# Performance work log

Measured on AMD Instinct MI355X. Metric: run time of the kernel, lower is better.

Reference implementation:

```python
import jax, jax.numpy as jnp
import numpy as np

N, L, I, H, D = 8192, 8, 256, 512, 8
PER = N // D  # nodes per depth level; level 0 nodes are tree roots


def setup_inputs() -> dict:
    key = jax.random.key(0)
    ks = jax.random.split(key, 9)
    s = 0.05
    x_seq = jax.random.normal(ks[0], (N, L, I), jnp.float32)
    # GRU params (torch nn.GRU layout, gate order r,z,n), stored transposed [in, 3H]
    W_ih = jax.random.normal(ks[1], (I, 3 * H), jnp.float32) * s
    W_hh = jax.random.normal(ks[2], (H, 3 * H), jnp.float32) * s
    b_ih = jax.random.normal(ks[3], (3 * H,), jnp.float32) * s
    b_hh = jax.random.normal(ks[4], (3 * H,), jnp.float32) * s
    # Child-sum TreeLSTM params: x-projections for i,o,u,f and recurrent U's
    Wx = jax.random.normal(ks[5], (H, 4 * H), jnp.float32) * s
    bx = jax.random.normal(ks[6], (4 * H,), jnp.float32) * s
    U_iou = jax.random.normal(ks[7], (H, 3 * H), jnp.float32) * s
    U_f = jax.random.normal(ks[8], (H, H), jnp.float32) * s
    # Forest structure: D levels of PER nodes; node at level d>0 has a random
    # parent at level d-1; roots (level 0) point at themselves (contribution is
    # zero because their own state is still zero when level 0 is processed).
    rng = np.random.default_rng(0)
    depth = np.repeat(np.arange(D), PER).astype(np.int32)
    parent = np.arange(N, dtype=np.int32)
    for d in range(1, D):
        parent[d * PER:(d + 1) * PER] = rng.integers((d - 1) * PER, d * PER, PER)
    root_ids = np.arange(PER, dtype=np.int32)
    return {
        "x_seq": x_seq, "W_ih": W_ih, "W_hh": W_hh, "b_ih": b_ih, "b_hh": b_hh,
        "Wx": Wx, "bx": bx, "U_iou": U_iou, "U_f": U_f,
        "parent": jnp.asarray(parent), "depth": jnp.asarray(depth),
        "root_ids": jnp.asarray(root_ids), "n_levels": D,
    }


def reference(x_seq, W_ih, W_hh, b_ih, b_hh, Wx, bx, U_iou, U_f,
              parent, depth, root_ids, n_levels):
    n = x_seq.shape[0]
    h_dim = W_hh.shape[0]

    # --- GRU over each node's encoding sequence (all nodes batched) ---
    def gru_step(h, x_t):  # h: [N,H], x_t: [N,I]
        gi = x_t @ W_ih + b_ih
        gh = h @ W_hh + b_hh
        ir, iz, inn = jnp.split(gi, 3, axis=-1)
        hr, hz, hn = jnp.split(gh, 3, axis=-1)
        r = jax.nn.sigmoid(ir + hr)
        z = jax.nn.sigmoid(iz + hz)
        ng = jnp.tanh(inn + r * hn)
        return (1.0 - z) * ng + z * h, None

    h0 = jnp.zeros((n, h_dim), x_seq.dtype)
    enc, _ = jax.lax.scan(gru_step, h0, jnp.swapaxes(x_seq, 0, 1))  # [N,H]

    # --- Child-sum TreeLSTM, processed leaves -> roots by depth level ---
    xg = enc @ Wx + bx  # [N,4H]
    xi, xo, xu, xf = jnp.split(xg, 4, axis=-1)
    c = jnp.zeros((n, h_dim), x_seq.dtype)
    h = jnp.zeros((n, h_dim), x_seq.dtype)
    for level in range(n_levels - 1, -1, -1):
        h_sum = jax.ops.segment_sum(h, parent, num_segments=n)  # sum over children
        giou = h_sum @ U_iou
        i = jax.nn.sigmoid(xi + giou[:, :h_dim])
        o = jax.nn.sigmoid(xo + giou[:, h_dim:2 * h_dim])
        u = jnp.tanh(xu + giou[:, 2 * h_dim:])
        # per-child forget gate uses parent's x projection and child's h
        f = jax.nn.sigmoid(xf[parent] + h @ U_f)
        fc = jax.ops.segment_sum(f * c, parent, num_segments=n)
        c_new = i * u + fc
        mask = (depth == level)[:, None]
        c = jnp.where(mask, c_new, c)
        h = jnp.where(mask, o * jnp.tanh(c_new), h)

    # root states per tree, stacked as [2, n_trees, H] -> (c_root, h_root)
    return jnp.stack([c[root_ids], h[root_ids]])
```

## Files before the change

kernel.cpp:

```cpp
#include <hip/hip_runtime.h>
#include <math.h>

typedef short bf16x8 __attribute__((ext_vector_type(8)));
typedef float f32x4 __attribute__((ext_vector_type(4)));

__device__ __forceinline__ float sigf(float x) { return 1.0f / (1.0f + __expf(-x)); }

__device__ __forceinline__ unsigned short f2bf(float f) {
    union { float f; unsigned u; } v; v.f = f;
    unsigned r = (v.u + 0x7FFFu + ((v.u >> 16) & 1u)) >> 16;
    return (unsigned short)r;
}
__device__ __forceinline__ float bf2f(unsigned short u) {
    union { unsigned u; float f; } v; v.u = ((unsigned)u) << 16; return v.f;
}

__device__ __forceinline__ void gload16(const unsigned short* g, unsigned short* l) {
    __builtin_amdgcn_global_load_lds(
        (const __attribute__((address_space(1))) void*)g,
        (__attribute__((address_space(3))) void*)l, 16, 0, 0);
}

__device__ __forceinline__ int swz(int slot, int row) {
    return (slot ^ ((row >> 1) & 3)) * 8;
}

__global__ void cvt_f32_bf16(const float* __restrict__ src,
                             unsigned short* __restrict__ dst, int n)
{
    const int i = (blockIdx.x * blockDim.x + threadIdx.x) * 4;
    if (i >= n) return;
    const float4 v = *reinterpret_cast<const float4*>(src + i);
    ushort4 o;
    o.x = f2bf(v.x); o.y = f2bf(v.y); o.z = f2bf(v.z); o.w = f2bf(v.w);
    *reinterpret_cast<ushort4*>(dst + i) = o;
}

__global__ void transpose_cvt(const float* __restrict__ src,
                              unsigned short* __restrict__ dst,
                              int rows, int cols)
{
    __shared__ float tile[32][33];
    const int bc = blockIdx.x * 32, br = blockIdx.y * 32;
    const int tx = threadIdx.x, ty = threadIdx.y;
    #pragma unroll
    for (int i = 0; i < 32; i += 8)
        tile[ty + i][tx] = src[(size_t)(br + ty + i) * cols + bc + tx];
    __syncthreads();
    #pragma unroll
    for (int i = 0; i < 32; i += 8)
        dst[(size_t)(bc + ty + i) * rows + br + tx] = f2bf(tile[tx][ty + i]);
}

__global__ __launch_bounds__(256)
void gru_mfma(const unsigned short* __restrict__ xb, int t,
              const unsigned short* __restrict__ hbi,
              unsigned short* __restrict__ hbo,
              const unsigned short* __restrict__ WihT,
              const unsigned short* __restrict__ WhhT,
              const float* __restrict__ b_ih, const float* __restrict__ b_hh)
{
    constexpr int I = 256, H = 512, LI = 2048;
    const int m0 = blockIdx.x * 128, j0 = blockIdx.y * 64;
    const int tid = (int)threadIdx.x, lane = tid & 63, wid = tid >> 6;
    const int wm = wid >> 1, wn = wid & 1;
    const int fr = lane & 15, kg = lane >> 4;
    const int lrow = lane >> 2;
    const int scol = swz(lane & 3, lrow);

    __shared__ unsigned short smem[3 * 10240];

    f32x4 ar[4][2], az[4][2], an[4][2], ah[4][2];
    #pragma unroll
    for (int i = 0; i < 4; ++i)
        #pragma unroll
        for (int j = 0; j < 2; ++j) {
            ar[i][j] = (f32x4){0.f, 0.f, 0.f, 0.f};
            az[i][j] = (f32x4){0.f, 0.f, 0.f, 0.f};
            an[i][j] = (f32x4){0.f, 0.f, 0.f, 0.f};
            ah[i][j] = (f32x4){0.f, 0.f, 0.f, 0.f};
        }

    constexpr int nkt1 = I / 32;
    constexpr int nkt = (I + H) / 32;

    auto stage = [&](int buf, int kt) {
        const bool s1 = (kt < nkt1);
        const int k0 = s1 ? kt * 32 : (kt - nkt1) * 32;
        unsigned short* base = &smem[buf * 10240];
        #pragma unroll
        for (int q = 0; q < 5; ++q) {
            const int c = wid * 5 + q;
            if (c < 8) {
                const int row = c * 16 + lrow;
                const unsigned short* g = s1
                    ? xb + (size_t)(m0 + row) * LI + t * I + k0 + scol
                    : hbi + (size_t)(m0 + row) * H + k0 + scol;
                gload16(g, base + c * 512);
            } else {
                const int bc = c - 8, gi = bc >> 2;
                const int row = (bc & 3) * 16 + lrow;
                const unsigned short* g = s1
                    ? WihT + (size_t)(gi * H + j0 + row) * I + k0 + scol
                    : WhhT + (size_t)(gi * H + j0 + row) * H + k0 + scol;
                gload16(g, base + c * 512);
            }
        }
    };

    stage(0, 0); stage(1, 1); stage(2, 2);
    int cur = 0;

    for (int kt = 0; kt < nkt; ++kt) {
        if (kt + 2 < nkt)      asm volatile("s_waitcnt vmcnt(10)" ::: "memory");
        else if (kt + 1 < nkt) asm volatile("s_waitcnt vmcnt(5)" ::: "memory");
        else                   asm volatile("s_waitcnt vmcnt(0)" ::: "memory");
        __builtin_amdgcn_s_barrier();

        const unsigned short* sb = &smem[cur * 10240];
        bf16x8 af[4], bfr[2], bfz[2], bfn[2];
        #pragma unroll
        for (int mi = 0; mi < 4; ++mi) {
            const int row = wm * 64 + mi * 16 + fr;
            af[mi] = *reinterpret_cast<const bf16x8*>(&sb[row * 32 + swz(kg, row)]);
        }
        #pragma unroll
        for (int ni = 0; ni < 2; ++ni) {
            const int row = wn * 32 + ni * 16 + fr;
            const int sw = swz(kg, row);
            bfr[ni] = *reinterpret_cast<const bf16x8*>(&sb[4096 + row * 32 + sw]);
            bfz[ni] = *reinterpret_cast<const bf16x8*>(&sb[4096 + (64 + row) * 32 + sw]);
            bfn[ni] = *reinterpret_cast<const bf16x8*>(&sb[4096 + (128 + row) * 32 + sw]);
        }
        const bool p1 = (kt < nkt1);
        #pragma unroll
        for (int mi = 0; mi < 4; ++mi)
            #pragma unroll
            for (int ni = 0; ni < 2; ++ni) {
                ar[mi][ni] = __builtin_amdgcn_mfma_f32_16x16x32_bf16(af[mi], bfr[ni], ar[mi][ni], 0, 0, 0);
                az[mi][ni] = __builtin_amdgcn_mfma_f32_16x16x32_bf16(af[mi], bfz[ni], az[mi][ni], 0, 0, 0);
                if (p1)
                    an[mi][ni] = __builtin_amdgcn_mfma_f32_16x16x32_bf16(af[mi], bfn[ni], an[mi][ni], 0, 0, 0);
                else
                    ah[mi][ni] = __builtin_amdgcn_mfma_f32_16x16x32_bf16(af[mi], bfn[ni], ah[mi][ni], 0, 0, 0);
            }

        asm volatile("s_waitcnt lgkmcnt(0)" ::: "memory");
        __builtin_amdgcn_s_barrier();
        if (kt + 3 < nkt) stage(cur, kt + 3);
        cur = (cur == 2) ? 0 : cur + 1;
    }

    #pragma unroll
    for (int ni = 0; ni < 2; ++ni) {
        const int j = j0 + wn * 32 + ni * 16 + fr;
        const float bir = b_ih[j],         bhr = b_hh[j];
        const float biz = b_ih[H + j],     bhz = b_hh[H + j];
        const float bin = b_ih[2 * H + j], bhn = b_hh[2 * H + j];
        #pragma unroll
        for (int mi = 0; mi < 4; ++mi) {
            #pragma unroll
            for (int r = 0; r < 4; ++r) {
                const int m = m0 + wm * 64 + mi * 16 + kg * 4 + r;
                const float rg = sigf(ar[mi][ni][r] + bir + bhr);
                const float zg = sigf(az[mi][ni][r] + biz + bhz);
                const float ng = tanhf(an[mi][ni][r] + bin + rg * (ah[mi][ni][r] + bhn));
                const size_t off = (size_t)m * H + j;
                const float hv = bf2f(hbi[off]);
                hbo[off] = f2bf((1.f - zg) * ng + zg * hv);
            }
        }
    }
}

__global__ __launch_bounds__(256)
void mfma_gemm128(const unsigned short* __restrict__ A,
                  const unsigned short* __restrict__ BT,
                  const float* __restrict__ bias,
                  float* __restrict__ C, int M, int N, int K)
{
    const int m0 = blockIdx.x * 128, n0 = blockIdx.y * 128;
    const int tid = (int)threadIdx.x, lane = tid & 63, wid = tid >> 6;
    const int wm = wid >> 1, wn = wid & 1;
    const int fr = lane & 15, kg = lane >> 4;
    const int lrow = lane >> 2;
    const int scol = swz(lane & 3, lrow);

    __shared__ unsigned short smem[3 * 8192];

    f32x4 acc[4][4];
    #pragma unroll
    for (int i = 0; i < 4; ++i)
        #pragma unroll
        for (int j = 0; j < 4; ++j)
            acc[i][j] = (f32x4){0.f, 0.f, 0.f, 0.f};

    auto stage = [&](int buf, int kt) {
        const int k0 = kt * 32;
        unsigned short* base = &smem[buf * 8192];
        #pragma unroll
        for (int q = 0; q < 4; ++q) {
            const int c = wid * 4 + q;
            const unsigned short* g = (c < 8)
                ? A + (size_t)(m0 + c * 16 + lrow) * K + k0 + scol
                : BT + (size_t)(n0 + (c - 8) * 16 + lrow) * K + k0 + scol;
            gload16(g, base + c * 512);
        }
    };

    const int nkt = K >> 5;
    stage(0, 0); stage(1, 1); stage(2, 2);
    int cur = 0;

    for (int kt = 0; kt < nkt; ++kt) {
        if (kt + 2 < nkt)      asm volatile("s_waitcnt vmcnt(8)" ::: "memory");
        else if (kt + 1 < nkt) asm volatile("s_waitcnt vmcnt(4)" ::: "memory");
        else                   asm volatile("s_waitcnt vmcnt(0)" ::: "memory");
        __builtin_amdgcn_s_barrier();

        const unsigned short* sb = &smem[cur * 8192];
        bf16x8 af[4], bf[4];
        #pragma unroll
        for (int mi = 0; mi < 4; ++mi) {
            const int row = wm * 64 + mi * 16 + fr;
            af[mi] = *reinterpret_cast<const bf16x8*>(&sb[row * 32 + swz(kg, row)]);
        }
        #pragma unroll
        for (int ni = 0; ni < 4; ++ni) {
            const int row = wn * 64 + ni * 16 + fr;
            bf[ni] = *reinterpret_cast<const bf16x8*>(&sb[4096 + row * 32 + swz(kg, row)]);
        }
        #pragma unroll
        for (int mi = 0; mi < 4; ++mi)
            #pragma unroll
            for (int ni = 0; ni < 4; ++ni)
                acc[mi][ni] = __builtin_amdgcn_mfma_f32_16x16x32_bf16(
                    af[mi], bf[ni], acc[mi][ni], 0, 0, 0);

        asm volatile("s_waitcnt lgkmcnt(0)" ::: "memory");
        __builtin_amdgcn_s_barrier();
        if (kt + 3 < nkt) stage(cur, kt + 3);
        cur = (cur == 2) ? 0 : cur + 1;
    }

    #pragma unroll
    for (int ni = 0; ni < 4; ++ni) {
        const int n = n0 + wn * 64 + ni * 16 + fr;
        const float bv = bias ? bias[n] : 0.f;
        #pragma unroll
        for (int mi = 0; mi < 4; ++mi)
            #pragma unroll
            for (int r = 0; r < 4; ++r) {
                const int m = m0 + wm * 64 + mi * 16 + kg * 4 + r;
                C[(size_t)m * N + n] = acc[mi][ni][r] + bv;
            }
    }
}

__global__ __launch_bounds__(256)
void tree_gemm(const unsigned short* __restrict__ hTb,
               const unsigned short* __restrict__ UcombT,
               const float* __restrict__ xg,
               const float* __restrict__ cT,
               const int* __restrict__ parent,
               int cstart, int pstart,
               float* __restrict__ giou,
               float* __restrict__ fcs)
{
    constexpr int H = 512, N4H = 2048, G3H = 1536;
    const int m0 = blockIdx.x * 64, n0 = blockIdx.y * 128;
    const int tid = (int)threadIdx.x, lane = tid & 63, wid = tid >> 6;
    const int wm = wid >> 1, wn = wid & 1;
    const int fr = lane & 15, kg = lane >> 4;
    const int lrow = lane >> 2;
    const int scol = swz(lane & 3, lrow);

    __shared__ unsigned short smem[3 * 6144];

    f32x4 acc[2][4];
    #pragma unroll
    for (int i = 0; i < 2; ++i)
        #pragma unroll
        for (int j = 0; j < 4; ++j)
            acc[i][j] = (f32x4){0.f, 0.f, 0.f, 0.f};

    auto stage = [&](int buf, int kt) {
        const int k0 = kt * 32;
        unsigned short* base = &smem[buf * 6144];
        #pragma unroll
        for (int q = 0; q < 3; ++q) {
            const int c = wid * 3 + q;
            const unsigned short* g = (c < 4)
                ? hTb + (size_t)(cstart + m0 + c * 16 + lrow) * H + k0 + scol
                : UcombT + (size_t)(n0 + (c - 4) * 16 + lrow) * H + k0 + scol;
            gload16(g, base + c * 512);
        }
    };

    constexpr int nkt = H / 32;
    stage(0, 0); stage(1, 1); stage(2, 2);
    int cur = 0;

    for (int kt = 0; kt < nkt; ++kt) {
        if (kt + 2 < nkt)      asm volatile("s_waitcnt vmcnt(6)" ::: "memory");
        else if (kt + 1 < nkt) asm volatile("s_waitcnt vmcnt(3)" ::: "memory");
        else                   asm volatile("s_waitcnt vmcnt(0)" ::: "memory");
        __builtin_amdgcn_s_barrier();

        const unsigned short* sb = &smem[cur * 6144];
        bf16x8 af[2], bf[4];
        #pragma unroll
        for (int mi = 0; mi < 2; ++mi) {
            const int row = wm * 32 + mi * 16 + fr;
            af[mi] = *reinterpret_cast<const bf16x8*>(&sb[row * 32 + swz(kg, row)]);
        }
        #pragma unroll
        for (int ni = 0; ni < 4; ++ni) {
            const int row = wn * 64 + ni * 16 + fr;
            bf[ni] = *reinterpret_cast<const bf16x8*>(&sb[2048 + row * 32 + swz(kg, row)]);
        }
        #pragma unroll
        for (int mi = 0; mi < 2; ++mi)
            #pragma unroll
            for (int ni = 0; ni < 4; ++ni)
                acc[mi][ni] = __builtin_amdgcn_mfma_f32_16x16x32_bf16(
                    af[mi], bf[ni], acc[mi][ni], 0, 0, 0);

        asm volatile("s_waitcnt lgkmcnt(0)" ::: "memory");
        __builtin_amdgcn_s_barrier();
        if (kt + 3 < nkt) stage(cur, kt + 3);
        cur = (cur == 2) ? 0 : cur + 1;
    }

    if (n0 < G3H) {
        #pragma unroll
        for (int mi = 0; mi < 2; ++mi)
            #pragma unroll
            for (int r = 0; r < 4; ++r) {
                const int m = m0 + wm * 32 + mi * 16 + kg * 4 + r;
                const int p = parent[cstart + m] - pstart;
                #pragma unroll
                for (int ni = 0; ni < 4; ++ni) {
                    const int n = n0 + wn * 64 + ni * 16 + fr;
                    atomicAdd(&giou[(size_t)p * G3H + n], acc[mi][ni][r]);
                }
            }
    } else {
        #pragma unroll
        for (int mi = 0; mi < 2; ++mi)
            #pragma unroll
            for (int r = 0; r < 4; ++r) {
                const int m = m0 + wm * 32 + mi * 16 + kg * 4 + r;
                const int child = cstart + m;
                const int p = parent[child];
                #pragma unroll
                for (int ni = 0; ni < 4; ++ni) {
                    const int jf = n0 + wn * 64 + ni * 16 + fr - G3H;
                    const float f = sigf(acc[mi][ni][r] + xg[(size_t)p * N4H + G3H + jf]);
                    atomicAdd(&fcs[(size_t)(p - pstart) * H + jf],
                              f * cT[(size_t)child * H + jf]);
                }
            }
    }
}

__global__ void level_update(const float* __restrict__ xg,
                             float* __restrict__ giou,
                             float* __restrict__ fcs,
                             float* __restrict__ cT, float* __restrict__ hT,
                             unsigned short* __restrict__ hb, int pstart)
{
    constexpr int H = 512, N4H = 2048, G3H = 1536;
    const int idx = blockIdx.x * blockDim.x + threadIdx.x;
    const int pi = idx >> 9, j = idx & (H - 1);
    const int p = pstart + pi;
    const size_t xb4 = (size_t)p * N4H;
    const size_t gb = (size_t)pi * G3H;
    const float ig = sigf(xg[xb4 + j] + giou[gb + j]);
    const float og = sigf(xg[xb4 + H + j] + giou[gb + H + j]);
    const float ug = tanhf(xg[xb4 + 2 * H + j] + giou[gb + 2 * H + j]);
    const float cn = ig * ug + fcs[idx];
    const float hn = og * tanhf(cn);
    const size_t off = (size_t)p * H + j;
    cT[off] = cn;
    hT[off] = hn;
    hb[off] = f2bf(hn);
    giou[gb + j] = 0.f;
    giou[gb + H + j] = 0.f;
    giou[gb + 2 * H + j] = 0.f;
    fcs[idx] = 0.f;
}

__global__ void gather_out_kernel(const float* __restrict__ c,
                                  const float* __restrict__ h,
                                  const int* __restrict__ root_ids,
                                  int nroot, float* __restrict__ out)
{
    constexpr int H = 512;
    const int idx = blockIdx.x * blockDim.x + threadIdx.x;
    const int t = idx >> 9, j = idx & (H - 1);
    const int rid = root_ids[t];
    out[idx] = c[(size_t)rid * H + j];
    out[(size_t)nroot * H + idx] = h[(size_t)rid * H + j];
}

extern "C" void kernel_launch(void* const* d_in, const int* in_sizes, int n_in,
                              void* d_out, int out_size, void* d_ws, size_t ws_size,
                              hipStream_t stream)
{
    const float* x_seq = (const float*)d_in[0];
    const float* W_ih  = (const float*)d_in[1];
    const float* W_hh  = (const float*)d_in[2];
    const float* b_ih  = (const float*)d_in[3];
    const float* b_hh  = (const float*)d_in[4];
    const float* Wx    = (const float*)d_in[5];
    const float* bx    = (const float*)d_in[6];
    const float* U_iou = (const float*)d_in[7];
    const float* U_f   = (const float*)d_in[8];
    const int* parent  = (const int*)d_in[9];
    const int* root_ids = (const int*)d_in[11];

    const int threeH = in_sizes[3];
    const int H   = threeH / 3;
    const int I   = in_sizes[1] / threeH;
    const int N   = in_sizes[9];
    const int L   = in_sizes[0] / (N * I);
    const int PER = in_sizes[11];
    const int D   = N / PER;

    const size_t NH = (size_t)N * H;
    const size_t PH = (size_t)PER * H;

    char* p = (char*)d_ws;
    const size_t zone_sz = ((size_t)N * 4 * H * 4 > (size_t)N * L * I * 2)
                         ? (size_t)N * 4 * H * 4 : (size_t)N * L * I * 2;
    unsigned short* xb = (unsigned short*)p;
    float* xg = (float*)p;                       p += zone_sz;
    unsigned short* hb0 = (unsigned short*)p;    p += NH * 2;
    unsigned short* hb1 = (unsigned short*)p;    p += NH * 2;
    float* cT = (float*)p;                       p += NH * 4;
    float* hT = (float*)p;                       p += NH * 4;
    unsigned short* WihT = (unsigned short*)p;   p += (size_t)threeH * I * 2;
    unsigned short* WhhT = (unsigned short*)p;   p += (size_t)threeH * H * 2;
    unsigned short* WxT  = (unsigned short*)p;   p += (size_t)4 * H * H * 2;
    unsigned short* UcombT = (unsigned short*)p; p += (size_t)4 * H * H * 2;
    float* giou = (float*)p;                     p += PH * 3 * 4;
    float* fcs  = (float*)p;                     p += PH * 4;
    if ((size_t)(p - (char*)d_ws) > ws_size) return;

    {
        const int n = N * L * I;
        cvt_f32_bf16<<<(n / 4 + 255) / 256, 256, 0, stream>>>(x_seq, xb, n);
        dim3 blk(32, 8);
        transpose_cvt<<<dim3(threeH / 32, I / 32), blk, 0, stream>>>(W_ih, WihT, I, threeH);
        transpose_cvt<<<dim3(threeH / 32, H / 32), blk, 0, stream>>>(W_hh, WhhT, H, threeH);
        transpose_cvt<<<dim3(4 * H / 32, H / 32), blk, 0, stream>>>(Wx, WxT, H, 4 * H);
        transpose_cvt<<<dim3(threeH / 32, H / 32), blk, 0, stream>>>(U_iou, UcombT, H, threeH);
        transpose_cvt<<<dim3(H / 32, H / 32), blk, 0, stream>>>(
            U_f, UcombT + (size_t)threeH * H, H, H);
    }
    hipMemsetAsync(hb0, 0, NH * 2, stream);
    hipMemsetAsync(giou, 0, PH * 4 * 4, stream);

    {
        dim3 grid(N / 128, H / 64);
        for (int t = 0; t < L; ++t) {
            const unsigned short* hin = (t & 1) ? hb1 : hb0;
            unsigned short* hout = (t & 1) ? hb0 : hb1;
            gru_mfma<<<grid, 256, 0, stream>>>(xb, t, hin, hout,
                                               WihT, WhhT, b_ih, b_hh);
        }
    }

    mfma_gemm128<<<dim3(N / 128, 4 * H / 128), 256, 0, stream>>>(
        hb0, WxT, bx, xg, N, 4 * H, H);

    unsigned short* hTb = hb1;
    const int pw_blocks = (int)(PH / 256);

    for (int lvl = D - 1; lvl >= 0; --lvl) {
        const int pstart = lvl * PER;
        const int cstart = (lvl + 1) * PER;

        if (lvl < D - 1)
            tree_gemm<<<dim3(PER / 64, (4 * H) / 128), 256, 0, stream>>>(
                hTb, UcombT, xg, cT, parent, cstart, pstart, giou, fcs);

        level_update<<<pw_blocks, 256, 0, stream>>>(xg, giou, fcs, cT, hT,
                                                    hTb, pstart);
    }

    gather_out_kernel<<<pw_blocks, 256, 0, stream>>>(cT, hT, root_ids, PER,
                                                     (float*)d_out);
}
```

Before: 541.5 us.

## Fuse GRU timesteps and tree levels into persistent kernels with grid barriers

The eight per-timestep GRU launches become one persistent kernel that loops over time. Blocks synchronize through a software grid barrier built on atomics, and the first input tiles for the next step are prefetched before the barrier. The per-level tree GEMM, level update and root gather are likewise merged into one persistent 256-block kernel with grid barriers between phases. Fast exp/rcp-based sigmoid and tanh replace the library calls. This removes about two dozen kernel launches and their gaps, but correctness now depends on every block being resident at once, and the fast tanh is slightly less accurate.

```diff
diff --git a/kernel.cpp b/kernel.cpp
--- a/kernel.cpp
+++ b/kernel.cpp
@@ -4,7 +4,13 @@
 typedef short bf16x8 __attribute__((ext_vector_type(8)));
 typedef float f32x4 __attribute__((ext_vector_type(4)));
 
-__device__ __forceinline__ float sigf(float x) { return 1.0f / (1.0f + __expf(-x)); }
+__device__ __forceinline__ float sigf(float x) {
+    return __builtin_amdgcn_rcpf(1.f + __expf(-x));
+}
+__device__ __forceinline__ float tanhf_fast(float x) {
+    const float e = __expf(2.f * x);
+    return 1.f - 2.f * __builtin_amdgcn_rcpf(e + 1.f);
+}
 
 __device__ __forceinline__ unsigned short f2bf(float f) {
     union { float f; unsigned u; } v; v.f = f;
@@ -23,6 +29,24 @@
 
 __device__ __forceinline__ int swz(int slot, int row) {
     return (slot ^ ((row >> 1) & 3)) * 8;
+}
+
+__device__ __forceinline__ void grid_sync(unsigned* cnt, unsigned* gen,
+                                          unsigned nb, unsigned my)
+{
+    __syncthreads();
+    if (threadIdx.x == 0) {
+        __threadfence();
+        if (atomicAdd(cnt, 1u) == nb - 1u) {
+            atomicExch(cnt, 0u);
+            __threadfence();
+            atomicExch(gen, my + 1u);
+        } else {
+            while (atomicAdd(gen, 0u) <= my) __builtin_amdgcn_s_sleep(2);
+        }
+        __threadfence();
+    }
+    __syncthreads();
 }
 
 __global__ void cvt_f32_bf16(const float* __restrict__ src,
@@ -52,16 +76,18 @@
         dst[(size_t)(bc + ty + i) * rows + br + tx] = f2bf(tile[tx][ty + i]);
 }
 
-__global__ __launch_bounds__(256)
-void gru_mfma(const unsigned short* __restrict__ xb, int t,
-              const unsigned short* __restrict__ hbi,
-              unsigned short* __restrict__ hbo,
-              const unsigned short* __restrict__ WihT,
-              const unsigned short* __restrict__ WhhT,
-              const float* __restrict__ b_ih, const float* __restrict__ b_hh)
+__global__ __launch_bounds__(256, 2)
+void gru_fused(const unsigned short* __restrict__ xb,
+               const unsigned short* __restrict__ WihT,
+               const unsigned short* __restrict__ WhhT,
+               const float* __restrict__ b_ih, const float* __restrict__ b_hh,
+               unsigned short* __restrict__ hb0,
+               unsigned short* __restrict__ hb1,
+               int L, unsigned* __restrict__ bar)
 {
     constexpr int I = 256, H = 512, LI = 2048;
-    const int m0 = blockIdx.x * 128, j0 = blockIdx.y * 64;
+    const int bx = blockIdx.x;
+    const int m0 = (bx >> 3) * 128, j0 = (bx & 7) * 64;
     const int tid = (int)threadIdx.x, lane = tid & 63, wid = tid >> 6;
     const int wm = wid >> 1, wn = wid & 1;
     const int fr = lane & 15, kg = lane >> 4;
@@ -70,21 +96,12 @@
 
     __shared__ unsigned short smem[3 * 10240];
 
-    f32x4 ar[4][2], az[4][2], an[4][2], ah[4][2];
-    #pragma unroll
-    for (int i = 0; i < 4; ++i)
-        #pragma unroll
-        for (int j = 0; j < 2; ++j) {
-            ar[i][j] = (f32x4){0.f, 0.f, 0.f, 0.f};
-            az[i][j] = (f32x4){0.f, 0.f, 0.f, 0.f};
-            an[i][j] = (f32x4){0.f, 0.f, 0.f, 0.f};
-            ah[i][j] = (f32x4){0.f, 0.f, 0.f, 0.f};
-        }
-
     constexpr int nkt1 = I / 32;
     constexpr int nkt = (I + H) / 32;
 
-    auto stage = [&](int buf, int kt) {
+    const unsigned short* hbi = hb0;
+
+    auto stage = [&](int buf, int kt, int tt) {
         const bool s1 = (kt < nkt1);
         const int k0 = s1 ? kt * 32 : (kt - nkt1) * 32;
         unsigned short* base = &smem[buf * 10240];
@@ -94,7 +111,7 @@
             if (c < 8) {
                 const int row = c * 16 + lrow;
                 const unsigned short* g = s1
-                    ? xb + (size_t)(m0 + row) * LI + t * I + k0 + scol
+                    ? xb + (size_t)(m0 + row) * LI + tt * I + k0 + scol
                     : hbi + (size_t)(m0 + row) * H + k0 + scol;
                 gload16(g, base + c * 512);
             } else {
@@ -108,68 +125,91 @@
         }
     };
 
-    stage(0, 0); stage(1, 1); stage(2, 2);
-    int cur = 0;
-
-    for (int kt = 0; kt < nkt; ++kt) {
-        if (kt + 2 < nkt)      asm volatile("s_waitcnt vmcnt(10)" ::: "memory");
-        else if (kt + 1 < nkt) asm volatile("s_waitcnt vmcnt(5)" ::: "memory");
-        else                   asm volatile("s_waitcnt vmcnt(0)" ::: "memory");
-        __builtin_amdgcn_s_barrier();
-
-        const unsigned short* sb = &smem[cur * 10240];
-        bf16x8 af[4], bfr[2], bfz[2], bfn[2];
-        #pragma unroll
-        for (int mi = 0; mi < 4; ++mi) {
-            const int row = wm * 64 + mi * 16 + fr;
-            af[mi] = *reinterpret_cast<const bf16x8*>(&sb[row * 32 + swz(kg, row)]);
-        }
+    stage(0, 0, 0); stage(1, 1, 0); stage(2, 2, 0);
+
+    for (int t = 0; t < L; ++t) {
+        hbi = (t & 1) ? hb1 : hb0;
+        unsigned short* hbo = (t & 1) ? hb0 : hb1;
+
+        f32x4 ar[4][2], az[4][2], an[4][2], ah[4][2];
+        #pragma unroll
+        for (int i = 0; i < 4; ++i)
+            #pragma unroll
+            for (int j = 0; j < 2; ++j) {
+                ar[i][j] = (f32x4){0.f, 0.f, 0.f, 0.f};
+                az[i][j] = (f32x4){0.f, 0.f, 0.f, 0.f};
+                an[i][j] = (f32x4){0.f, 0.f, 0.f, 0.f};
+                ah[i][j] = (f32x4){0.f, 0.f, 0.f, 0.f};
+            }
+
+        int cur = 0;
+        for (int kt = 0; kt < nkt; ++kt) {
+            if (kt + 2 < nkt)      asm volatile("s_waitcnt vmcnt(10)" ::: "memory");
+            else if (kt + 1 < nkt) asm volatile("s_waitcnt vmcnt(5)" ::: "memory");
+            else                   asm volatile("s_waitcnt vmcnt(0)" ::: "memory");
+            __builtin_amdgcn_s_barrier();
+
+            const unsigned short* sb = &smem[cur * 10240];
+            bf16x8 af[4], bfr[2], bfz[2], bfn[2];
+            #pragma unroll
+            for (int mi = 0; mi < 4; ++mi) {
+                const int row = wm * 64 + mi * 16 + fr;
+                af[mi] = *reinterpret_cast<const bf16x8*>(&sb[row * 32 + swz(kg, row)]);
+            }
+            #pragma unroll
+            for (int ni = 0; ni < 2; ++ni) {
+                const int row = wn * 32 + ni * 16 + fr;
+                const int sw = swz(kg, row);
+                bfr[ni] = *reinterpret_cast<const bf16x8*>(&sb[4096 + (row) * 32 + sw]);
+                bfz[ni] = *reinterpret_cast<const bf16x8*>(&sb[4096 + (64 + row) * 32 + sw]);
+                bfn[ni] = *reinterpret_cast<const bf16x8*>(&sb[4096 + (128 + row) * 32 + sw]);
+            }
+            const bool p1 = (kt < nkt1);
+            #pragma unroll
+            for (int mi = 0; mi < 4; ++mi)
+                #pragma unroll
+                for (int ni = 0; ni < 2; ++ni) {
+                    ar[mi][ni] = __builtin_amdgcn_mfma_f32_16x16x32_bf16(af[mi], bfr[ni], ar[mi][ni], 0, 0, 0);
+                    az[mi][ni] = __builtin_amdgcn_mfma_f32_16x16x32_bf16(af[mi], bfz[ni], az[mi][ni], 0, 0, 0);
+                    if (p1)
+                        an[mi][ni] = __builtin_amdgcn_mfma_f32_16x16x32_bf16(af[mi], bfn[ni], an[mi][ni], 0, 0, 0);
+                    else
+                        ah[mi][ni] = __builtin_amdgcn_mfma_f32_16x16x32_bf16(af[mi], bfn[ni], ah[mi][ni], 0, 0, 0);
+                }
+
+            asm volatile("s_waitcnt lgkmcnt(0)" ::: "memory");
+            __builtin_amdgcn_s_barrier();
+            if (kt + 3 < nkt) stage(cur, kt + 3, t);
+            cur = (cur == 2) ? 0 : cur + 1;
+        }
+
+        if (t + 1 < L) {
+            stage(0, 0, t + 1); stage(1, 1, t + 1); stage(2, 2, t + 1);
+        }
+
         #pragma unroll
         for (int ni = 0; ni < 2; ++ni) {
-            const int row = wn * 32 + ni * 16 + fr;
-            const int sw = swz(kg, row);
-            bfr[ni] = *reinterpret_cast<const bf16x8*>(&sb[4096 + row * 32 + sw]);
-            bfz[ni] = *reinterpret_cast<const bf16x8*>(&sb[4096 + (64 + row) * 32 + sw]);
-            bfn[ni] = *reinterpret_cast<const bf16x8*>(&sb[4096 + (128 + row) * 32 + sw]);
-        }
-        const bool p1 = (kt < nkt1);
-        #pragma unroll
-        for (int mi = 0; mi < 4; ++mi)
-            #pragma unroll
-            for (int ni = 0; ni < 2; ++ni) {
-                ar[mi][ni] = __builtin_amdgcn_mfma_f32_16x16x32_bf16(af[mi], bfr[ni], ar[mi][ni], 0, 0, 0);
-                az[mi][ni] = __builtin_amdgcn_mfma_f32_16x16x32_bf16(af[mi], bfz[ni], az[mi][ni], 0, 0, 0);
-                if (p1)
-                    an[mi][ni] = __builtin_amdgcn_mfma_f32_16x16x32_bf16(af[mi], bfn[ni], an[mi][ni], 0, 0, 0);
-                else
-                    ah[mi][ni] = __builtin_amdgcn_mfma_f32_16x16x32_bf16(af[mi], bfn[ni], ah[mi][ni], 0, 0, 0);
-            }
-
-        asm volatile("s_waitcnt lgkmcnt(0)" ::: "memory");
-        __builtin_amdgcn_s_barrier();
-        if (kt + 3 < nkt) stage(cur, kt + 3);
-        cur = (cur == 2) ? 0 : cur + 1;
-    }
-
-    #pragma unroll
-    for (int ni = 0; ni < 2; ++ni) {
-        const int j = j0 + wn * 32 + ni * 16 + fr;
-        const float bir = b_ih[j],         bhr = b_hh[j];
-        const float biz = b_ih[H + j],     bhz = b_hh[H + j];
-        const float bin = b_ih[2 * H + j], bhn = b_hh[2 * H + j];
-        #pragma unroll
-        for (int mi = 0; mi < 4; ++mi) {
-            #pragma unroll
-            for (int r = 0; r < 4; ++r) {
-                const int m = m0 + wm * 64 + mi * 16 + kg * 4 + r;
-                const float rg = sigf(ar[mi][ni][r] + bir + bhr);
-                const float zg = sigf(az[mi][ni][r] + biz + bhz);
-                const float ng = tanhf(an[mi][ni][r] + bin + rg * (ah[mi][ni][r] + bhn));
-                const size_t off = (size_t)m * H + j;
-                const float hv = bf2f(hbi[off]);
-                hbo[off] = f2bf((1.f - zg) * ng + zg * hv);
-            }
-        }
+            const int j = j0 + wn * 32 + ni * 16 + fr;
+            const float bir = b_ih[j],         bhr = b_hh[j];
+            const float biz = b_ih[H + j],     bhz = b_hh[H + j];
+            const float bin = b_ih[2 * H + j], bhn = b_hh[2 * H + j];
+            #pragma unroll
+            for (int mi = 0; mi < 4; ++mi) {
+                #pragma unroll
+                for (int r = 0; r < 4; ++r) {
+                    const int m = m0 + wm * 64 + mi * 16 + kg * 4 + r;
+                    const float rg = sigf(ar[mi][ni][r] + bir + bhr);
+                    const float zg = sigf(az[mi][ni][r] + biz + bhz);
+                    const float ng = tanhf_fast(an[mi][ni][r] + bin + rg * (ah[mi][ni][r] + bhn));
+                    const size_t off = (size_t)m * H + j;
+                    const float hv = bf2f(hbi[off]);
+                    hbo[off] = f2bf((1.f - zg) * ng + zg * hv);
+                }
+            }
+        }
+
+        if (t + 1 < L)
+            grid_sync(&bar[0], &bar[1], gridDim.x, (unsigned)t);
     }
 }
 
@@ -257,151 +297,158 @@
     }
 }
 
-__global__ __launch_bounds__(256)
-void tree_gemm(const unsigned short* __restrict__ hTb,
-               const unsigned short* __restrict__ UcombT,
-               const float* __restrict__ xg,
-               const float* __restrict__ cT,
-               const int* __restrict__ parent,
-               int cstart, int pstart,
-               float* __restrict__ giou,
-               float* __restrict__ fcs)
+__global__ __launch_bounds__(256, 1)
+void tree_fused(unsigned short* __restrict__ hb,
+                const unsigned short* __restrict__ UcombT,
+                const float* __restrict__ xg,
+                float* __restrict__ cT, float* __restrict__ hT,
+                const int* __restrict__ parent,
+                const int* __restrict__ root_ids,
+                float* __restrict__ giou,
+                float* __restrict__ fcs,
+                float* __restrict__ out,
+                int D, int PER, unsigned* __restrict__ bar)
 {
     constexpr int H = 512, N4H = 2048, G3H = 1536;
-    const int m0 = blockIdx.x * 64, n0 = blockIdx.y * 128;
-    const int tid = (int)threadIdx.x, lane = tid & 63, wid = tid >> 6;
+    const int bx = (int)blockIdx.x, tid = (int)threadIdx.x;
+    const int lane = tid & 63, wid = tid >> 6;
     const int wm = wid >> 1, wn = wid & 1;
     const int fr = lane & 15, kg = lane >> 4;
     const int lrow = lane >> 2;
     const int scol = swz(lane & 3, lrow);
+    const int per_blk = PER * H / 256;
 
     __shared__ unsigned short smem[3 * 6144];
 
-    f32x4 acc[2][4];
+    unsigned my = 0;
+
+    for (int lvl = D - 1; lvl >= 0; --lvl) {
+        const int pstart = lvl * PER;
+        const int cstart = (lvl + 1) * PER;
+
+        if (lvl < D - 1) {
+            const int m0 = (bx >> 4) * 64, n0 = (bx & 15) * 128;
+
+            f32x4 acc[2][4];
+            #pragma unroll
+            for (int i = 0; i < 2; ++i)
+                #pragma unroll
+                for (int j = 0; j < 4; ++j)
+                    acc[i][j] = (f32x4){0.f, 0.f, 0.f, 0.f};
+
+            auto stage = [&](int buf, int kt) {
+                const int k0 = kt * 32;
+                unsigned short* base = &smem[buf * 6144];
+                #pragma unroll
+                for (int q = 0; q < 3; ++q) {
+                    const int c = wid * 3 + q;
+                    const unsigned short* g = (c < 4)
+                        ? hb + (size_t)(cstart + m0 + c * 16 + lrow) * H + k0 + scol
+                        : UcombT + (size_t)(n0 + (c - 4) * 16 + lrow) * H + k0 + scol;
+                    gload16(g, base + c * 512);
+                }
+            };
+
+            constexpr int nkt = H / 32;
+            stage(0, 0); stage(1, 1); stage(2, 2);
+            int cur = 0;
+
+            for (int kt = 0; kt < nkt; ++kt) {
+                if (kt + 2 < nkt)      asm volatile("s_waitcnt vmcnt(6)" ::: "memory");
+                else if (kt + 1 < nkt) asm volatile("s_waitcnt vmcnt(3)" ::: "memory");
+                else                   asm volatile("s_waitcnt vmcnt(0)" ::: "memory");
+                __builtin_amdgcn_s_barrier();
+
+                const unsigned short* sb = &smem[cur * 6144];
+                bf16x8 af[2], bf[4];
+                #pragma unroll
+                for (int mi = 0; mi < 2; ++mi) {
+                    const int row = wm * 32 + mi * 16 + fr;
+                    af[mi] = *reinterpret_cast<const bf16x8*>(&sb[row * 32 + swz(kg, row)]);
+                }
+                #pragma unroll
+                for (int ni = 0; ni < 4; ++ni) {
+                    const int row = wn * 64 + ni * 16 + fr;
+                    bf[ni] = *reinterpret_cast<const bf16x8*>(&sb[2048 + row * 32 + swz(kg, row)]);
+                }
+                #pragma unroll
+                for (int mi = 0; mi < 2; ++mi)
+                    #pragma unroll
+                    for (int ni = 0; ni < 4; ++ni)
+                        acc[mi][ni] = __builtin_amdgcn_mfma_f32_16x16x32_bf16(
+                            af[mi], bf[ni], acc[mi][ni], 0, 0, 0);
+
+                asm volatile("s_waitcnt lgkmcnt(0)" ::: "memory");
+                __builtin_amdgcn_s_barrier();
+                if (kt + 3 < nkt) stage(cur, kt + 3);
+                cur = (cur == 2) ? 0 : cur + 1;
+            }
+
+            if (n0 < G3H) {
+                #pragma unroll
+                for (int mi = 0; mi < 2; ++mi)
+                    #pragma unroll
+                    for (int r = 0; r < 4; ++r) {
+                        const int m = m0 + wm * 32 + mi * 16 + kg * 4 + r;
+                        const int p = parent[cstart + m] - pstart;
+                        #pragma unroll
+                        for (int ni = 0; ni < 4; ++ni) {
+                            const int n = n0 + wn * 64 + ni * 16 + fr;
+                            atomicAdd(&giou[(size_t)p * G3H + n], acc[mi][ni][r]);
+                        }
+                    }
+            } else {
+                #pragma unroll
+                for (int mi = 0; mi < 2; ++mi)
+                    #pragma unroll
+                    for (int r = 0; r < 4; ++r) {
+                        const int m = m0 + wm * 32 + mi * 16 + kg * 4 + r;
+                        const int child = cstart + m;
+                        const int p = parent[child];
+                        #pragma unroll
+                        for (int ni = 0; ni < 4; ++ni) {
+                            const int jf = n0 + wn * 64 + ni * 16 + fr - G3H;
+                            const float f = sigf(acc[mi][ni][r] + xg[(size_t)p * N4H + G3H + jf]);
+                            atomicAdd(&fcs[(size_t)(p - pstart) * H + jf],
+                                      f * cT[(size_t)child * H + jf]);
+                        }
+                    }
+            }
+            grid_sync(&bar[0], &bar[1], gridDim.x, my++);
+        }
+
+        #pragma unroll
+        for (int e = 0; e < 8; ++e) {
+            const int idx = bx * per_blk + e * 256 + tid;
+            const int pi = idx >> 9, j = idx & (H - 1);
+            const int p = pstart + pi;
+            const size_t xb4 = (size_t)p * N4H;
+            const size_t gb = (size_t)pi * G3H;
+            const float ig = sigf(xg[xb4 + j] + giou[gb + j]);
+            const float og = sigf(xg[xb4 + H + j] + giou[gb + H + j]);
+            const float ug = tanhf_fast(xg[xb4 + 2 * H + j] + giou[gb + 2 * H + j]);
+            const float cn = ig * ug + fcs[idx];
+            const float hn = og * tanhf_fast(cn);
+            const size_t off = (size_t)p * H + j;
+            cT[off] = cn;
+            hT[off] = hn;
+            hb[off] = f2bf(hn);
+            giou[gb + j] = 0.f;
+            giou[gb + H + j] = 0.f;
+            giou[gb + 2 * H + j] = 0.f;
+            fcs[idx] = 0.f;
+        }
+        grid_sync(&bar[0], &bar[1], gridDim.x, my++);
+    }
+
     #pragma unroll
-    for (int i = 0; i < 2; ++i)
-        #pragma unroll
-        for (int j = 0; j < 4; ++j)
-            acc[i][j] = (f32x4){0.f, 0.f, 0.f, 0.f};
-
-    auto stage = [&](int buf, int kt) {
-        const int k0 = kt * 32;
-        unsigned short* base = &smem[buf * 6144];
-        #pragma unroll
-        for (int q = 0; q < 3; ++q) {
-            const int c = wid * 3 + q;
-            const unsigned short* g = (c < 4)
-                ? hTb + (size_t)(cstart + m0 + c * 16 + lrow) * H + k0 + scol
-                : UcombT + (size_t)(n0 + (c - 4) * 16 + lrow) * H + k0 + scol;
-            gload16(g, base + c * 512);
-        }
-    };
-
-    constexpr int nkt = H / 32;
-    stage(0, 0); stage(1, 1); stage(2, 2);
-    int cur = 0;
-
-    for (int kt = 0; kt < nkt; ++kt) {
-        if (kt + 2 < nkt)      asm volatile("s_waitcnt vmcnt(6)" ::: "memory");
-        else if (kt + 1 < nkt) asm volatile("s_waitcnt vmcnt(3)" ::: "memory");
-        else                   asm volatile("s_waitcnt vmcnt(0)" ::: "memory");
-        __builtin_amdgcn_s_barrier();
-
-        const unsigned short* sb = &smem[cur * 6144];
-        bf16x8 af[2], bf[4];
-        #pragma unroll
-        for (int mi = 0; mi < 2; ++mi) {
-            const int row = wm * 32 + mi * 16 + fr;
-            af[mi] = *reinterpret_cast<const bf16x8*>(&sb[row * 32 + swz(kg, row)]);
-        }
-        #pragma unroll
-        for (int ni = 0; ni < 4; ++ni) {
-            const int row = wn * 64 + ni * 16 + fr;
-            bf[ni] = *reinterpret_cast<const bf16x8*>(&sb[2048 + row * 32 + swz(kg, row)]);
-        }
-        #pragma unroll
-        for (int mi = 0; mi < 2; ++mi)
-            #pragma unroll
-            for (int ni = 0; ni < 4; ++ni)
-                acc[mi][ni] = __builtin_amdgcn_mfma_f32_16x16x32_bf16(
-                    af[mi], bf[ni], acc[mi][ni], 0, 0, 0);
-
-        asm volatile("s_waitcnt lgkmcnt(0)" ::: "memory");
-        __builtin_amdgcn_s_barrier();
-        if (kt + 3 < nkt) stage(cur, kt + 3);
-        cur = (cur == 2) ? 0 : cur + 1;
-    }
-
-    if (n0 < G3H) {
-        #pragma unroll
-        for (int mi = 0; mi < 2; ++mi)
-            #pragma unroll
-            for (int r = 0; r < 4; ++r) {
-                const int m = m0 + wm * 32 + mi * 16 + kg * 4 + r;
-                const int p = parent[cstart + m] - pstart;
-                #pragma unroll
-                for (int ni = 0; ni < 4; ++ni) {
-                    const int n = n0 + wn * 64 + ni * 16 + fr;
-                    atomicAdd(&giou[(size_t)p * G3H + n], acc[mi][ni][r]);
-                }
-            }
-    } else {
-        #pragma unroll
-        for (int mi = 0; mi < 2; ++mi)
-            #pragma unroll
-            for (int r = 0; r < 4; ++r) {
-                const int m = m0 + wm * 32 + mi * 16 + kg * 4 + r;
-                const int child = cstart + m;
-                const int p = parent[child];
-                #pragma unroll
-                for (int ni = 0; ni < 4; ++ni) {
-                    const int jf = n0 + wn * 64 + ni * 16 + fr - G3H;
-                    const float f = sigf(acc[mi][ni][r] + xg[(size_t)p * N4H + G3H + jf]);
-                    atomicAdd(&fcs[(size_t)(p - pstart) * H + jf],
-                              f * cT[(size_t)child * H + jf]);
-                }
-            }
-    }
-}
-
-__global__ void level_update(const float* __restrict__ xg,
-                             float* __restrict__ giou,
-                             float* __restrict__ fcs,
-                             float* __restrict__ cT, float* __restrict__ hT,
-                             unsigned short* __restrict__ hb, int pstart)
-{
-    constexpr int H = 512, N4H = 2048, G3H = 1536;
-    const int idx = blockIdx.x * blockDim.x + threadIdx.x;
-    const int pi = idx >> 9, j = idx & (H - 1);
-    const int p = pstart + pi;
-    const size_t xb4 = (size_t)p * N4H;
-    const size_t gb = (size_t)pi * G3H;
-    const float ig = sigf(xg[xb4 + j] + giou[gb + j]);
-    const float og = sigf(xg[xb4 + H + j] + giou[gb + H + j]);
-    const float ug = tanhf(xg[xb4 + 2 * H + j] + giou[gb + 2 * H + j]);
-    const float cn = ig * ug + fcs[idx];
-    const float hn = og * tanhf(cn);
-    const size_t off = (size_t)p * H + j;
-    cT[off] = cn;
-    hT[off] = hn;
-    hb[off] = f2bf(hn);
-    giou[gb + j] = 0.f;
-    giou[gb + H + j] = 0.f;
-    giou[gb + 2 * H + j] = 0.f;
-    fcs[idx] = 0.f;
-}
-
-__global__ void gather_out_kernel(const float* __restrict__ c,
-                                  const float* __restrict__ h,
-                                  const int* __restrict__ root_ids,
-                                  int nroot, float* __restrict__ out)
-{
-    constexpr int H = 512;
-    const int idx = blockIdx.x * blockDim.x + threadIdx.x;
-    const int t = idx >> 9, j = idx & (H - 1);
-    const int rid = root_ids[t];
-    out[idx] = c[(size_t)rid * H + j];
-    out[(size_t)nroot * H + idx] = h[(size_t)rid * H + j];
+    for (int e = 0; e < 8; ++e) {
+        const int idx = bx * per_blk + e * 256 + tid;
+        const int tt = idx >> 9, j = idx & (H - 1);
+        const int rid = root_ids[tt];
+        out[idx] = cT[(size_t)rid * H + j];
+        out[(size_t)PER * H + idx] = hT[(size_t)rid * H + j];
+    }
 }
 
 extern "C" void kernel_launch(void* const* d_in, const int* in_sizes, int n_in,
@@ -446,6 +493,7 @@
     unsigned short* UcombT = (unsigned short*)p; p += (size_t)4 * H * H * 2;
     float* giou = (float*)p;                     p += PH * 3 * 4;
     float* fcs  = (float*)p;                     p += PH * 4;
+    unsigned* bar = (unsigned*)p;                p += 512;
     if ((size_t)(p - (char*)d_ws) > ws_size) return;
 
     {
@@ -461,35 +509,15 @@
     }
     hipMemsetAsync(hb0, 0, NH * 2, stream);
     hipMemsetAsync(giou, 0, PH * 4 * 4, stream);
-
-    {
-        dim3 grid(N / 128, H / 64);
-        for (int t = 0; t < L; ++t) {
-            const unsigned short* hin = (t & 1) ? hb1 : hb0;
-            unsigned short* hout = (t & 1) ? hb0 : hb1;
-            gru_mfma<<<grid, 256, 0, stream>>>(xb, t, hin, hout,
-                                               WihT, WhhT, b_ih, b_hh);
-        }
-    }
+    hipMemsetAsync(bar, 0, 512, stream);
+
+    gru_fused<<<(N / 128) * (H / 64), 256, 0, stream>>>(
+        xb, WihT, WhhT, b_ih, b_hh, hb0, hb1, L, bar);
 
     mfma_gemm128<<<dim3(N / 128, 4 * H / 128), 256, 0, stream>>>(
         hb0, WxT, bx, xg, N, 4 * H, H);
 
-    unsigned short* hTb = hb1;
-    const int pw_blocks = (int)(PH / 256);
-
-    for (int lvl = D - 1; lvl >= 0; --lvl) {
-        const int pstart = lvl * PER;
-        const int cstart = (lvl + 1) * PER;
-
-        if (lvl < D - 1)
-            tree_gemm<<<dim3(PER / 64, (4 * H) / 128), 256, 0, stream>>>(
-                hTb, UcombT, xg, cT, parent, cstart, pstart, giou, fcs);
-
-        level_update<<<pw_blocks, 256, 0, stream>>>(xg, giou, fcs, cT, hT,
-                                                    hTb, pstart);
-    }
-
-    gather_out_kernel<<<pw_blocks, 256, 0, stream>>>(cT, hT, root_ids, PER,
-                                                     (float*)d_out);
-}
+    tree_fused<<<256, 256, 0, stream>>>(hb1, UcombT, xg, cT, hT, parent,
+                                        root_ids, giou, fcs, (float*)d_out,
+                                        D, PER, bar + 64);
+}
```

Result: slower. 1.318 ms (+143.4%).
